# Kernel optimization log

Hardware: AMD Instinct MI355X
Metric: run time of the kernel (lower is better)

The kernel has to match this reference:

```python
import jax, jax.numpy as jnp
import numpy as np

B, L, H, E, MODES = 32, 2048, 8, 64, 64
SCALE = 1.0 / (512 * 512)  # 1/(in_channels*out_channels)


def setup_inputs() -> dict:
    key = jax.random.key(0)
    kq, kk, kv, kwr, kwi = jax.random.split(key, 5)
    # frequency mode selection: shuffled range(L//2), first MODES, sorted (get_frequency_modes)
    rng = np.random.default_rng(0)
    index = np.sort(rng.permutation(L // 2)[:MODES]).astype(np.int32)
    return {
        "q": jax.random.normal(kq, (B, L, H, E), dtype=jnp.float32),
        "k": jax.random.normal(kk, (B, L, H, E), dtype=jnp.float32),
        "v": jax.random.normal(kv, (B, L, H, E), dtype=jnp.float32),
        "w_real": SCALE * jax.random.uniform(kwr, (H, E, E, MODES), dtype=jnp.float32),
        "w_imag": SCALE * jax.random.uniform(kwi, (H, E, E, MODES), dtype=jnp.float32),
        "index": jnp.asarray(index),
    }


def reference(q, k, v, w_real, w_imag, index):
    # q: [B, L, H, E]; k, v unused by FourierBlock
    Bq, Lq, Hq, Eq = q.shape
    x = jnp.transpose(q, (0, 2, 3, 1))            # [B, H, E, L]
    x_ft = jnp.fft.rfft(x, axis=-1)               # [B, H, E, L//2+1] complex
    xs = jnp.take(x_ft, index, axis=-1)           # gather selected modes: [B, H, E, M]
    W = w_real + 1j * w_imag                      # [H, E, E, M] complex
    # vectorized per-mode complex einsum ('bhi,hio->bho' over all modes m)
    out = jnp.einsum('bhim,hiom->bhom', xs, W)    # [B, H, E, M]
    n_freq = Lq // 2 + 1
    # original writes mode wi into slot wi (0..M-1), rest stay zero
    out_ft = jnp.concatenate(
        [out, jnp.zeros((Bq, Hq, Eq, n_freq - out.shape[-1]), dtype=out.dtype)], axis=-1)
    return jnp.fft.irfft(out_ft, n=Lq, axis=-1)   # [B, H, E, L] real
```

## Files before the change

kernel.cpp:

```cpp
#include <hip/hip_runtime.h>
#include <math.h>

#define NB 32
#define NL 2048
#define NH 8
#define NE 64
#define NM 64
#define MRI 128
#define BK 128
#define NCH 16

typedef __attribute__((ext_vector_type(8))) __bf16 bf16x8;
typedef __attribute__((ext_vector_type(2))) __bf16 bf16x2;
typedef __attribute__((ext_vector_type(8))) unsigned short us8;
typedef __attribute__((ext_vector_type(4))) unsigned short us4;
typedef __attribute__((ext_vector_type(4))) float f32x4;
typedef __attribute__((ext_vector_type(16))) float f32x16;

__device__ __forceinline__ unsigned short f2bf(float x) {
  unsigned int u = __builtin_bit_cast(unsigned int, x);
  u = (u + 0x7fffu + ((u >> 16) & 1u)) >> 16;
  return (unsigned short)u;
}
__device__ __forceinline__ float bf2f(unsigned short u) {
  return __builtin_bit_cast(float, (unsigned int)u << 16);
}
__device__ __forceinline__ unsigned int pk2(float lo, float hi) {
  bf16x2 v;
  v[0] = (__bf16)lo;
  v[1] = (__bf16)hi;
  return __builtin_bit_cast(unsigned int, v);
}
__device__ __forceinline__ void gll16(const void* g, void* l) {
  __builtin_amdgcn_global_load_lds(
      (const __attribute__((address_space(1))) void*)g,
      (__attribute__((address_space(3))) void*)l, 16, 0, 0);
}

__global__ void tables_k(const int* __restrict__ idx,
                         const float* __restrict__ wr, const float* __restrict__ wi,
                         unsigned short* __restrict__ T, unsigned short* __restrict__ IT,
                         unsigned short* __restrict__ WBr, unsigned short* __restrict__ WBi) {
  int gid = blockIdx.x * blockDim.x + threadIdx.x;
  const float w0 = 6.283185307179586f / (float)NL;
  {
    int row = gid >> 11, l = gid & (NL - 1);
    int m = row & 63;
    int f = idx[m];
    float s, c;
    sincosf((float)((f * l) & (NL - 1)) * w0, &s, &c);
    T[gid] = f2bf(row < 64 ? c : -s);
  }
  {
    int lp = gid >> 7, k = gid & 127;
    int m = k & 63;
    float s, c;
    sincosf((float)((m * lp) & (NL - 1)) * w0, &s, &c);
    float v = (k < 64) ? ((m == 0 ? 1.0f : 2.0f) / (float)NL) * c
                       : (m == 0 ? 0.0f : (-2.0f / (float)NL) * s);
    IT[gid] = f2bf(v);
  }
  {
    const float2* wr2 = (const float2*)wr;
    const float2* wi2 = (const float2*)wi;
    unsigned int* obr = (unsigned int*)WBr;
    unsigned int* obi = (unsigned int*)WBi;
#pragma unroll
    for (int r = 0; r < 4; ++r) {
      int j = r * 262144 + gid;
      float2 a = wr2[j];
      float2 b2 = wi2[j];
      obr[j] = pk2(a.x, a.y);
      obi[j] = pk2(b2.x, b2.y);
    }
  }
}

__global__ __launch_bounds__(1024) void fused_k(const float* __restrict__ q,
                                                const unsigned short* __restrict__ T,
                                                const unsigned short* __restrict__ IT,
                                                const unsigned short* __restrict__ WBr,
                                                const unsigned short* __restrict__ WBi,
                                                float* __restrict__ out) {
  __shared__ __align__(16) char smem[99328];
  int t = threadIdx.x, lane = t & 63, wid = t >> 6;
  int h = blockIdx.x & 7, b = blockIdx.x >> 3;

  {
    char* Ab = smem;
    char* B0 = smem + 65536;
    char* B1 = smem + 65536 + 16896;
    const float* qb = q + ((size_t)b * NL * NH + h) * NE;
    int tm = wid & 3;
    int te = (wid >> 2) & 1;
    int kh = wid >> 3;
    int eq = t & 15, lq = t >> 4;
    f32x16 acc32 = {};
    f32x4 qA[2], qB[2];

    auto qload = [&](int c, f32x4* qr) {
#pragma unroll
      for (int p = 0; p < 2; ++p)
        qr[p] = *(const f32x4*)(qb + (size_t)(c * BK + lq * 2 + p) * (NH * NE) + eq * 4);
    };
    auto writesB = [&](const f32x4* qr, char* bb) {
#pragma unroll
      for (int j = 0; j < 4; ++j) {
        int e = eq * 4 + j;
        *(unsigned int*)(bb + e * 264 + lq * 4) = pk2(qr[0][j], qr[1][j]);
      }
    };
    auto stageA = [&](int bufi, int c) {
#pragma unroll
      for (int n = 0; n < 2; ++n) {
        int lin = n * 16384 + t * 16;
        int row = lin >> 8;
        int colb = (lin & 255) ^ ((row & 7) << 4);
        gll16((const char*)T + (size_t)row * (NL * 2) + (size_t)c * 256 + colb,
              Ab + bufi * 32768 + lin);
      }
    };
    auto compute = [&](const char* ab, const char* bb) {
#pragma unroll
      for (int ks = 0; ks < 4; ++ks) {
        int k0 = (kh * 4 + ks) * 16;
        int e = te * 32 + (lane & 31);
        int boff = e * 264 + (k0 + (lane >> 5) * 8) * 2;
        uint2 blo = *(const uint2*)(bb + boff);
        uint2 bhi = *(const uint2*)(bb + boff + 8);
        bf16x8 bfr = __builtin_bit_cast(bf16x8, make_uint4(blo.x, blo.y, bhi.x, bhi.y));
        int row = tm * 32 + (lane & 31);
        int aoff = (row * 256 + (k0 + (lane >> 5) * 8) * 2) ^ ((row & 7) << 4);
        bf16x8 afr = __builtin_bit_cast(bf16x8, *(const us8*)(ab + aoff));
        acc32 = __builtin_amdgcn_mfma_f32_32x32x16_bf16(afr, bfr, acc32, 0, 0, 0);
      }
    };

    qload(0, qA);
    qload(1, qB);
    stageA(0, 0);
    writesB(qA, B0);
    asm volatile("s_waitcnt vmcnt(0)" ::: "memory");
    __builtin_amdgcn_sched_barrier(0);
    asm volatile("s_waitcnt lgkmcnt(0)" ::: "memory");
    __builtin_amdgcn_s_barrier();
    for (int c = 0; c < 14; c += 2) {
      stageA(1, c + 1);
      qload(c + 2, qA);
      compute(Ab, B0);
      asm volatile("s_waitcnt vmcnt(2)" ::: "memory");
      __builtin_amdgcn_sched_barrier(0);
      __builtin_amdgcn_s_barrier();
      writesB(qB, B1);
      asm volatile("s_waitcnt lgkmcnt(0)" ::: "memory");
      __builtin_amdgcn_s_barrier();

      stageA(0, c + 2);
      qload(c + 3, qB);
      compute(Ab + 32768, B1);
      asm volatile("s_waitcnt vmcnt(2)" ::: "memory");
      __builtin_amdgcn_sched_barrier(0);
      __builtin_amdgcn_s_barrier();
      writesB(qA, B0);
      asm volatile("s_waitcnt lgkmcnt(0)" ::: "memory");
      __builtin_amdgcn_s_barrier();
    }
    stageA(1, 15);
    compute(Ab, B0);
    asm volatile("s_waitcnt vmcnt(0)" ::: "memory");
    __builtin_amdgcn_sched_barrier(0);
    __builtin_amdgcn_s_barrier();
    writesB(qB, B1);
    asm volatile("s_waitcnt lgkmcnt(0)" ::: "memory");
    __builtin_amdgcn_s_barrier();
    compute(Ab + 32768, B1);
    __syncthreads();

    float* scr = (float*)(smem + 65536);
    int tile = wid & 7;
    if (kh == 1) {
#pragma unroll
      for (int r = 0; r < 16; ++r) {
        int row = (r & 3) + 8 * (r >> 2) + 4 * (lane >> 5);
        scr[tile * 1024 + row * 32 + (lane & 31)] = acc32[r];
      }
    }
    __syncthreads();
    if (kh == 0) {
#pragma unroll
      for (int r = 0; r < 16; ++r) {
        int row = (r & 3) + 8 * (r >> 2) + 4 * (lane >> 5);
        float v = acc32[r] + scr[tile * 1024 + row * 32 + (lane & 31)];
        int grow = tm * 32 + row;
        int gcol = te * 32 + (lane & 31);
        int off = (grow * 272 + gcol * 4) ^ (((grow >> 3) & 7) << 4);
        *(float*)(smem + off) = v;
      }
    }
  }
  __syncthreads();

  {
    char* OtB = smem + 34816;
    int o = t >> 4, mq = t & 15;
    const unsigned short* wbr = WBr + (size_t)h * 262144 + o * 64 + mq * 4;
    const unsigned short* wbi = WBi + (size_t)h * 262144 + o * 64 + mq * 4;
    float orr[4] = {}, oii[4] = {};
#pragma unroll 2
    for (int ib = 0; ib < 16; ++ib) {
      f32x4 xr4[4], xi4[4];
#pragma unroll
      for (int mi = 0; mi < 4; ++mi) {
        int m = mq * 4 + mi;
        xr4[mi] = *(const f32x4*)(smem + ((m * 272 + ib * 16) ^ (((m >> 3) & 7) << 4)));
        xi4[mi] = *(const f32x4*)(smem + (((64 + m) * 272 + ib * 16) ^ (((m >> 3) & 7) << 4)));
      }
      us4 wr4[4], wi4[4];
#pragma unroll
      for (int ii = 0; ii < 4; ++ii) {
        int i = ib * 4 + ii;
        wr4[ii] = *(const us4*)(wbr + (size_t)i * 4096);
        wi4[ii] = *(const us4*)(wbi + (size_t)i * 4096);
      }
#pragma unroll
      for (int ii = 0; ii < 4; ++ii)
#pragma unroll
        for (int mi = 0; mi < 4; ++mi) {
          float wrv = bf2f(wr4[ii][mi]);
          float wiv = bf2f(wi4[ii][mi]);
          orr[mi] += xr4[mi][ii] * wrv - xi4[mi][ii] * wiv;
          oii[mi] += xr4[mi][ii] * wiv + xi4[mi][ii] * wrv;
        }
    }
    uint2 vr = make_uint2(pk2(orr[0], orr[1]), pk2(orr[2], orr[3]));
    uint2 vi = make_uint2(pk2(oii[0], oii[1]), pk2(oii[2], oii[3]));
    *(uint2*)(OtB + ((o * 256 + mq * 8) ^ ((o & 7) << 4))) = vr;
    *(uint2*)(OtB + ((o * 256 + 128 + mq * 8) ^ ((o & 7) << 4))) = vi;
  }
  __syncthreads();

  {
    const char* OtB = smem + 34816;
    bf16x8 af[2][8];
#pragma unroll
    for (int rg2 = 0; rg2 < 2; ++rg2)
#pragma unroll
      for (int ks = 0; ks < 8; ++ks) {
        int row = rg2 * 32 + (lane & 31);
        int off = (row * 256 + ks * 32 + (lane >> 5) * 16) ^ ((row & 7) << 4);
        af[rg2][ks] = __builtin_bit_cast(bf16x8, *(const us8*)(OtB + off));
      }
    float* ob = out + ((size_t)(b * 8 + h) * 64) * NL;
    int l0 = wid * 128;
    for (int ct = 0; ct < 4; ++ct) {
      int lr = l0 + ct * 32 + (lane & 31);
      f32x16 a2[2] = {};
#pragma unroll
      for (int ks = 0; ks < 8; ++ks) {
        bf16x8 bv = __builtin_bit_cast(
            bf16x8, *(const us8*)(IT + (size_t)lr * MRI + ks * 16 + (lane >> 5) * 8));
        a2[0] = __builtin_amdgcn_mfma_f32_32x32x16_bf16(af[0][ks], bv, a2[0], 0, 0, 0);
        a2[1] = __builtin_amdgcn_mfma_f32_32x32x16_bf16(af[1][ks], bv, a2[1], 0, 0, 0);
      }
#pragma unroll
      for (int rg2 = 0; rg2 < 2; ++rg2)
#pragma unroll
        for (int rg = 0; rg < 16; ++rg) {
          int row = rg2 * 32 + ((rg & 3) + 8 * (rg >> 2) + 4 * (lane >> 5));
          ob[(size_t)row * NL + lr] = a2[rg2][rg];
        }
    }
  }
}

extern "C" void kernel_launch(void* const* d_in, const int* in_sizes, int n_in,
                              void* d_out, int out_size, void* d_ws, size_t ws_size,
                              hipStream_t stream) {
  const float* q = (const float*)d_in[0];
  const float* wr = (const float*)d_in[3];
  const float* wi = (const float*)d_in[4];
  const int* idx = (const int*)d_in[5];
  float* out = (float*)d_out;
  char* ws = (char*)d_ws;

  constexpr size_t TBYTES = (size_t)MRI * NL * 2;
  constexpr size_t WBBYTES = (size_t)NH * NE * NE * NM * 2;
  constexpr size_t NEED = 2 * TBYTES + 2 * WBBYTES;
  if (ws_size < NEED) return;

  unsigned short* T = (unsigned short*)ws;
  unsigned short* IT = (unsigned short*)(ws + TBYTES);
  unsigned short* WBr = (unsigned short*)(ws + 2 * TBYTES);
  unsigned short* WBi = (unsigned short*)(ws + 2 * TBYTES + WBBYTES);

  hipLaunchKernelGGL(tables_k, dim3(1024), dim3(256), 0, stream, idx, wr, wi, T, IT, WBr, WBi);
  hipLaunchKernelGGL(fused_k, dim3(NB * NH), dim3(1024), 0, stream, q, T, IT, WBr, WBi, out);
}
```

Measured before the change: 85.36 us.

## Pre-swizzle DFT table into MFMA fragment order and load A into registers

```diff
diff --git a/kernel.cpp b/kernel.cpp
--- a/kernel.cpp
+++ b/kernel.cpp
@@ -31,25 +31,23 @@
   v[1] = (__bf16)hi;
   return __builtin_bit_cast(unsigned int, v);
 }
-__device__ __forceinline__ void gll16(const void* g, void* l) {
-  __builtin_amdgcn_global_load_lds(
-      (const __attribute__((address_space(1))) void*)g,
-      (__attribute__((address_space(3))) void*)l, 16, 0, 0);
-}
 
 __global__ void tables_k(const int* __restrict__ idx,
                          const float* __restrict__ wr, const float* __restrict__ wi,
-                         unsigned short* __restrict__ T, unsigned short* __restrict__ IT,
+                         unsigned short* __restrict__ Tf, unsigned short* __restrict__ IT,
                          unsigned short* __restrict__ WBr, unsigned short* __restrict__ WBi) {
   int gid = blockIdx.x * blockDim.x + threadIdx.x;
   const float w0 = 6.283185307179586f / (float)NL;
   {
-    int row = gid >> 11, l = gid & (NL - 1);
+    int j = gid & 7, lane_ = (gid >> 3) & 63, tm_ = (gid >> 9) & 3;
+    int ks_ = (gid >> 11) & 3, kh_ = (gid >> 13) & 1, c_ = gid >> 14;
+    int row = tm_ * 32 + (lane_ & 31);
     int m = row & 63;
+    int k = c_ * 128 + kh_ * 64 + ks_ * 16 + (lane_ >> 5) * 8 + j;
     int f = idx[m];
-    float s, c;
-    sincosf((float)((f * l) & (NL - 1)) * w0, &s, &c);
-    T[gid] = f2bf(row < 64 ? c : -s);
+    float s, c2;
+    sincosf((float)((f * k) & (NL - 1)) * w0, &s, &c2);
+    Tf[gid] = f2bf(row < 64 ? c2 : -s);
   }
   {
     int lp = gid >> 7, k = gid & 127;
@@ -82,14 +80,13 @@
                                                 const unsigned short* __restrict__ WBr,
                                                 const unsigned short* __restrict__ WBi,
                                                 float* __restrict__ out) {
-  __shared__ __align__(16) char smem[99328];
+  __shared__ __align__(16) char smem[84992];
   int t = threadIdx.x, lane = t & 63, wid = t >> 6;
   int h = blockIdx.x & 7, b = blockIdx.x >> 3;
 
   {
-    char* Ab = smem;
-    char* B0 = smem + 65536;
-    char* B1 = smem + 65536 + 16896;
+    char* B0 = smem + 51200;
+    char* B1 = smem + 51200 + 16896;
     const float* qb = q + ((size_t)b * NL * NH + h) * NE;
     int tm = wid & 3;
     int te = (wid >> 2) & 1;
@@ -97,6 +94,7 @@
     int eq = t & 15, lq = t >> 4;
     f32x16 acc32 = {};
     f32x4 qA[2], qB[2];
+    us8 arA[4], arB[4];
 
     auto qload = [&](int c, f32x4* qr) {
 #pragma unroll
@@ -110,17 +108,12 @@
         *(unsigned int*)(bb + e * 264 + lq * 4) = pk2(qr[0][j], qr[1][j]);
       }
     };
-    auto stageA = [&](int bufi, int c) {
-#pragma unroll
-      for (int n = 0; n < 2; ++n) {
-        int lin = n * 16384 + t * 16;
-        int row = lin >> 8;
-        int colb = (lin & 255) ^ ((row & 7) << 4);
-        gll16((const char*)T + (size_t)row * (NL * 2) + (size_t)c * 256 + colb,
-              Ab + bufi * 32768 + lin);
-      }
-    };
-    auto compute = [&](const char* ab, const char* bb) {
+    auto loadAreg = [&](int c, us8* ar) {
+#pragma unroll
+      for (int ks = 0; ks < 4; ++ks)
+        ar[ks] = *(const us8*)(T + ((((size_t)c * 2 + kh) * 4 + ks) * 4 + tm) * 512 + lane * 8);
+    };
+    auto compute = [&](const us8* ar, const char* bb) {
 #pragma unroll
       for (int ks = 0; ks < 4; ++ks) {
         int k0 = (kh * 4 + ks) * 16;
@@ -129,54 +122,38 @@
         uint2 blo = *(const uint2*)(bb + boff);
         uint2 bhi = *(const uint2*)(bb + boff + 8);
         bf16x8 bfr = __builtin_bit_cast(bf16x8, make_uint4(blo.x, blo.y, bhi.x, bhi.y));
-        int row = tm * 32 + (lane & 31);
-        int aoff = (row * 256 + (k0 + (lane >> 5) * 8) * 2) ^ ((row & 7) << 4);
-        bf16x8 afr = __builtin_bit_cast(bf16x8, *(const us8*)(ab + aoff));
-        acc32 = __builtin_amdgcn_mfma_f32_32x32x16_bf16(afr, bfr, acc32, 0, 0, 0);
+        acc32 = __builtin_amdgcn_mfma_f32_32x32x16_bf16(
+            __builtin_bit_cast(bf16x8, ar[ks]), bfr, acc32, 0, 0, 0);
       }
     };
 
     qload(0, qA);
     qload(1, qB);
-    stageA(0, 0);
+    loadAreg(0, arA);
     writesB(qA, B0);
-    asm volatile("s_waitcnt vmcnt(0)" ::: "memory");
-    __builtin_amdgcn_sched_barrier(0);
     asm volatile("s_waitcnt lgkmcnt(0)" ::: "memory");
     __builtin_amdgcn_s_barrier();
-    for (int c = 0; c < 14; c += 2) {
-      stageA(1, c + 1);
-      qload(c + 2, qA);
-      compute(Ab, B0);
-      asm volatile("s_waitcnt vmcnt(2)" ::: "memory");
-      __builtin_amdgcn_sched_barrier(0);
+    for (int c = 0; c < 16; c += 2) {
+      loadAreg(c + 1, arB);
+      if (c + 2 < 16) qload(c + 2, qA);
+      compute(arA, B0);
       __builtin_amdgcn_s_barrier();
       writesB(qB, B1);
       asm volatile("s_waitcnt lgkmcnt(0)" ::: "memory");
       __builtin_amdgcn_s_barrier();
-
-      stageA(0, c + 2);
-      qload(c + 3, qB);
-      compute(Ab + 32768, B1);
-      asm volatile("s_waitcnt vmcnt(2)" ::: "memory");
-      __builtin_amdgcn_sched_barrier(0);
-      __builtin_amdgcn_s_barrier();
-      writesB(qA, B0);
-      asm volatile("s_waitcnt lgkmcnt(0)" ::: "memory");
-      __builtin_amdgcn_s_barrier();
-    }
-    stageA(1, 15);
-    compute(Ab, B0);
-    asm volatile("s_waitcnt vmcnt(0)" ::: "memory");
-    __builtin_amdgcn_sched_barrier(0);
-    __builtin_amdgcn_s_barrier();
-    writesB(qB, B1);
-    asm volatile("s_waitcnt lgkmcnt(0)" ::: "memory");
-    __builtin_amdgcn_s_barrier();
-    compute(Ab + 32768, B1);
+      if (c + 2 < 16) loadAreg(c + 2, arA);
+      if (c + 3 < 16) qload(c + 3, qB);
+      compute(arB, B1);
+      if (c + 2 < 16) {
+        __builtin_amdgcn_s_barrier();
+        writesB(qA, B0);
+        asm volatile("s_waitcnt lgkmcnt(0)" ::: "memory");
+        __builtin_amdgcn_s_barrier();
+      }
+    }
     __syncthreads();
 
-    float* scr = (float*)(smem + 65536);
+    float* scr = (float*)(smem + 51200);
     int tile = wid & 7;
     if (kh == 1) {
 #pragma unroll
@@ -288,11 +265,11 @@
   constexpr size_t NEED = 2 * TBYTES + 2 * WBBYTES;
   if (ws_size < NEED) return;
 
-  unsigned short* T = (unsigned short*)ws;
+  unsigned short* Tf = (unsigned short*)ws;
   unsigned short* IT = (unsigned short*)(ws + TBYTES);
   unsigned short* WBr = (unsigned short*)(ws + 2 * TBYTES);
   unsigned short* WBi = (unsigned short*)(ws + 2 * TBYTES + WBBYTES);
 
-  hipLaunchKernelGGL(tables_k, dim3(1024), dim3(256), 0, stream, idx, wr, wi, T, IT, WBr, WBi);
-  hipLaunchKernelGGL(fused_k, dim3(NB * NH), dim3(1024), 0, stream, q, T, IT, WBr, WBi, out);
-}
+  hipLaunchKernelGGL(tables_k, dim3(1024), dim3(256), 0, stream, idx, wr, wi, Tf, IT, WBr, WBi);
+  hipLaunchKernelGGL(fused_k, dim3(NB * NH), dim3(1024), 0, stream, q, Tf, IT, WBr, WBi, out);
+}
```

Result: slower. 93.87 us (+10.0%).

## Split fused kernel into mode-halved DFT/mix kernel and tiled inverse-DFT GEMM kernel

Applied to the files above, without the earlier changes.

```diff
diff --git a/kernel.cpp b/kernel.cpp
--- a/kernel.cpp
+++ b/kernel.cpp
@@ -76,48 +76,49 @@
   }
 }
 
-__global__ __launch_bounds__(1024) void fused_k(const float* __restrict__ q,
+__global__ __launch_bounds__(512) void dftmix_k(const float* __restrict__ q,
                                                 const unsigned short* __restrict__ T,
-                                                const unsigned short* __restrict__ IT,
                                                 const unsigned short* __restrict__ WBr,
                                                 const unsigned short* __restrict__ WBi,
-                                                float* __restrict__ out) {
-  __shared__ __align__(16) char smem[99328];
+                                                unsigned short* __restrict__ O) {
+  __shared__ __align__(16) char smem[66560];
   int t = threadIdx.x, lane = t & 63, wid = t >> 6;
-  int h = blockIdx.x & 7, b = blockIdx.x >> 3;
-
-  {
-    char* Ab = smem;
-    char* B0 = smem + 65536;
-    char* B1 = smem + 65536 + 16896;
+  int h = blockIdx.x & 7, mh2 = (blockIdx.x >> 3) & 1, b = blockIdx.x >> 4;
+
+  {
+    char* A0 = smem;
+    char* A1 = smem + 16384;
+    char* B0 = smem + 32768;
+    char* B1 = smem + 32768 + 16896;
     const float* qb = q + ((size_t)b * NL * NH + h) * NE;
-    int tm = wid & 3;
-    int te = (wid >> 2) & 1;
-    int kh = wid >> 3;
-    int eq = t & 15, lq = t >> 4;
+    int tm = wid & 1;
+    int te = (wid >> 1) & 1;
+    int kh = wid >> 2;
+    int eq = t & 15, ls = t >> 4;
     f32x16 acc32 = {};
-    f32x4 qA[2], qB[2];
+    f32x4 qA[4], qB[4];
 
     auto qload = [&](int c, f32x4* qr) {
 #pragma unroll
-      for (int p = 0; p < 2; ++p)
-        qr[p] = *(const f32x4*)(qb + (size_t)(c * BK + lq * 2 + p) * (NH * NE) + eq * 4);
+      for (int p = 0; p < 4; ++p)
+        qr[p] = *(const f32x4*)(qb + (size_t)(c * BK + ls * 4 + p) * (NH * NE) + eq * 4);
     };
     auto writesB = [&](const f32x4* qr, char* bb) {
 #pragma unroll
       for (int j = 0; j < 4; ++j) {
         int e = eq * 4 + j;
-        *(unsigned int*)(bb + e * 264 + lq * 4) = pk2(qr[0][j], qr[1][j]);
+        *(uint2*)(bb + e * 264 + ls * 8) =
+            make_uint2(pk2(qr[0][j], qr[1][j]), pk2(qr[2][j], qr[3][j]));
       }
     };
-    auto stageA = [&](int bufi, int c) {
+    auto stageA = [&](char* ab, int c) {
 #pragma unroll
       for (int n = 0; n < 2; ++n) {
-        int lin = n * 16384 + t * 16;
-        int row = lin >> 8;
-        int colb = (lin & 255) ^ ((row & 7) << 4);
-        gll16((const char*)T + (size_t)row * (NL * 2) + (size_t)c * 256 + colb,
-              Ab + bufi * 32768 + lin);
+        int lin = n * 8192 + t * 16;
+        int rl = lin >> 8;
+        int grow = (rl < 32) ? (mh2 * 32 + rl) : (64 + mh2 * 32 + rl - 32);
+        int colb = (lin & 255) ^ ((rl & 7) << 4);
+        gll16((const char*)T + (size_t)grow * (NL * 2) + (size_t)c * 256 + colb, ab + lin);
       }
     };
     auto compute = [&](const char* ab, const char* bb) {
@@ -136,48 +137,46 @@
       }
     };
 
+    stageA(A0, 0);
     qload(0, qA);
     qload(1, qB);
-    stageA(0, 0);
     writesB(qA, B0);
-    asm volatile("s_waitcnt vmcnt(0)" ::: "memory");
-    __builtin_amdgcn_sched_barrier(0);
     asm volatile("s_waitcnt lgkmcnt(0)" ::: "memory");
     __builtin_amdgcn_s_barrier();
     for (int c = 0; c < 14; c += 2) {
-      stageA(1, c + 1);
+      stageA(A1, c + 1);
       qload(c + 2, qA);
-      compute(Ab, B0);
-      asm volatile("s_waitcnt vmcnt(2)" ::: "memory");
+      compute(A0, B0);
+      asm volatile("s_waitcnt vmcnt(4)" ::: "memory");
       __builtin_amdgcn_sched_barrier(0);
       __builtin_amdgcn_s_barrier();
       writesB(qB, B1);
       asm volatile("s_waitcnt lgkmcnt(0)" ::: "memory");
       __builtin_amdgcn_s_barrier();
 
-      stageA(0, c + 2);
-      qload(c + 3, qB);
-      compute(Ab + 32768, B1);
-      asm volatile("s_waitcnt vmcnt(2)" ::: "memory");
+      stageA(A0, c + 2);
+      if (c + 3 < 16) qload(c + 3, qB);
+      compute(A1, B1);
+      asm volatile("s_waitcnt vmcnt(4)" ::: "memory");
       __builtin_amdgcn_sched_barrier(0);
       __builtin_amdgcn_s_barrier();
       writesB(qA, B0);
       asm volatile("s_waitcnt lgkmcnt(0)" ::: "memory");
       __builtin_amdgcn_s_barrier();
     }
-    stageA(1, 15);
-    compute(Ab, B0);
+    stageA(A1, 15);
+    compute(A0, B0);
     asm volatile("s_waitcnt vmcnt(0)" ::: "memory");
     __builtin_amdgcn_sched_barrier(0);
     __builtin_amdgcn_s_barrier();
     writesB(qB, B1);
     asm volatile("s_waitcnt lgkmcnt(0)" ::: "memory");
     __builtin_amdgcn_s_barrier();
-    compute(Ab + 32768, B1);
+    compute(A1, B1);
     __syncthreads();
 
-    float* scr = (float*)(smem + 65536);
-    int tile = wid & 7;
+    float* scr = (float*)(smem + 32768);
+    int tile = wid & 3;
     if (kh == 1) {
 #pragma unroll
       for (int r = 0; r < 16; ++r) {
@@ -201,19 +200,20 @@
   __syncthreads();
 
   {
-    char* OtB = smem + 34816;
-    int o = t >> 4, mq = t & 15;
-    const unsigned short* wbr = WBr + (size_t)h * 262144 + o * 64 + mq * 4;
-    const unsigned short* wbi = WBi + (size_t)h * 262144 + o * 64 + mq * 4;
+    int o = t >> 3, mq = t & 7;
+    int mgbase = mh2 * 32 + mq * 4;
+    const unsigned short* wbr = WBr + (size_t)h * 262144 + o * 64 + mgbase;
+    const unsigned short* wbi = WBi + (size_t)h * 262144 + o * 64 + mgbase;
     float orr[4] = {}, oii[4] = {};
 #pragma unroll 2
     for (int ib = 0; ib < 16; ++ib) {
       f32x4 xr4[4], xi4[4];
 #pragma unroll
       for (int mi = 0; mi < 4; ++mi) {
-        int m = mq * 4 + mi;
-        xr4[mi] = *(const f32x4*)(smem + ((m * 272 + ib * 16) ^ (((m >> 3) & 7) << 4)));
-        xi4[mi] = *(const f32x4*)(smem + (((64 + m) * 272 + ib * 16) ^ (((m >> 3) & 7) << 4)));
+        int ml = mq * 4 + mi;
+        xr4[mi] = *(const f32x4*)(smem + ((ml * 272 + ib * 16) ^ (((ml >> 3) & 7) << 4)));
+        xi4[mi] = *(const f32x4*)(smem +
+                                  (((32 + ml) * 272 + ib * 16) ^ ((((32 + ml) >> 3) & 7) << 4)));
       }
       us4 wr4[4], wi4[4];
 #pragma unroll
@@ -232,45 +232,68 @@
           oii[mi] += xr4[mi][ii] * wiv + xi4[mi][ii] * wrv;
         }
     }
-    uint2 vr = make_uint2(pk2(orr[0], orr[1]), pk2(orr[2], orr[3]));
-    uint2 vi = make_uint2(pk2(oii[0], oii[1]), pk2(oii[2], oii[3]));
-    *(uint2*)(OtB + ((o * 256 + mq * 8) ^ ((o & 7) << 4))) = vr;
-    *(uint2*)(OtB + ((o * 256 + 128 + mq * 8) ^ ((o & 7) << 4))) = vi;
+    unsigned short* ob = O + (((size_t)b * 8 + h) * 64 + o) * MRI;
+    *(uint2*)(ob + mgbase) = make_uint2(pk2(orr[0], orr[1]), pk2(orr[2], orr[3]));
+    *(uint2*)(ob + 64 + mgbase) = make_uint2(pk2(oii[0], oii[1]), pk2(oii[2], oii[3]));
+  }
+}
+
+__global__ __launch_bounds__(256) void idft_k(const unsigned short* __restrict__ O,
+                                              const unsigned short* __restrict__ IT,
+                                              float* __restrict__ out) {
+  int bid = blockIdx.x;
+  int ct = bid & 15, rt = (bid >> 4) & 3, b = bid >> 6;
+  int t = threadIdx.x, lane = t & 63, wid = t >> 6;
+  __shared__ unsigned short Als[128 * 128];
+  __shared__ unsigned short Bls[128 * 128];
+  const unsigned short* Og = O + ((size_t)b * 512 + rt * 128) * MRI;
+  const unsigned short* Ig = IT + (size_t)ct * 128 * MRI;
+#pragma unroll
+  for (int n = 0; n < 8; ++n) {
+    int lin = n * 4096 + wid * 1024 + lane * 16;
+    int row = lin >> 8;
+    int colb = (lin & 255) ^ ((row & 7) << 4);
+    gll16((const char*)Og + (size_t)row * 256 + colb, (char*)Als + n * 4096 + wid * 1024);
+  }
+#pragma unroll
+  for (int n = 0; n < 8; ++n) {
+    int lin = n * 4096 + wid * 1024 + lane * 16;
+    int row = lin >> 8;
+    int colb = (lin & 255) ^ ((row & 7) << 4);
+    gll16((const char*)Ig + (size_t)row * 256 + colb, (char*)Bls + n * 4096 + wid * 1024);
   }
   __syncthreads();
-
-  {
-    const char* OtB = smem + 34816;
-    bf16x8 af[2][8];
-#pragma unroll
-    for (int rg2 = 0; rg2 < 2; ++rg2)
-#pragma unroll
-      for (int ks = 0; ks < 8; ++ks) {
-        int row = rg2 * 32 + (lane & 31);
-        int off = (row * 256 + ks * 32 + (lane >> 5) * 16) ^ ((row & 7) << 4);
-        af[rg2][ks] = __builtin_bit_cast(bf16x8, *(const us8*)(OtB + off));
-      }
-    float* ob = out + ((size_t)(b * 8 + h) * 64) * NL;
-    int l0 = wid * 128;
-    for (int ct = 0; ct < 4; ++ct) {
-      int lr = l0 + ct * 32 + (lane & 31);
-      f32x16 a2[2] = {};
-#pragma unroll
-      for (int ks = 0; ks < 8; ++ks) {
-        bf16x8 bv = __builtin_bit_cast(
-            bf16x8, *(const us8*)(IT + (size_t)lr * MRI + ks * 16 + (lane >> 5) * 8));
-        a2[0] = __builtin_amdgcn_mfma_f32_32x32x16_bf16(af[0][ks], bv, a2[0], 0, 0, 0);
-        a2[1] = __builtin_amdgcn_mfma_f32_32x32x16_bf16(af[1][ks], bv, a2[1], 0, 0, 0);
-      }
-#pragma unroll
-      for (int rg2 = 0; rg2 < 2; ++rg2)
-#pragma unroll
-        for (int rg = 0; rg < 16; ++rg) {
-          int row = rg2 * 32 + ((rg & 3) + 8 * (rg >> 2) + 4 * (lane >> 5));
-          ob[(size_t)row * NL + lr] = a2[rg2][rg];
-        }
-    }
-  }
+  int wr2 = (wid >> 1) * 64, wc = (wid & 1) * 64;
+  f32x16 acc[2][2] = {};
+#pragma unroll
+  for (int ksp = 0; ksp < 8; ++ksp) {
+    bf16x8 af[2], bfv[2];
+#pragma unroll
+    for (int i2 = 0; i2 < 2; ++i2) {
+      int row = wr2 + i2 * 32 + (lane & 31);
+      int off = ((row << 8) + (ksp << 5) + ((lane >> 5) << 4)) ^ ((row & 7) << 4);
+      af[i2] = __builtin_bit_cast(bf16x8, *(const us8*)((const char*)Als + off));
+      int nr = wc + i2 * 32 + (lane & 31);
+      int off2 = ((nr << 8) + (ksp << 5) + ((lane >> 5) << 4)) ^ ((nr & 7) << 4);
+      bfv[i2] = __builtin_bit_cast(bf16x8, *(const us8*)((const char*)Bls + off2));
+    }
+#pragma unroll
+    for (int i2 = 0; i2 < 2; ++i2)
+#pragma unroll
+      for (int j2 = 0; j2 < 2; ++j2)
+        acc[i2][j2] = __builtin_amdgcn_mfma_f32_32x32x16_bf16(af[i2], bfv[j2], acc[i2][j2], 0, 0, 0);
+  }
+  float* ob = out + ((size_t)b * 512 + rt * 128) * NL + ct * 128;
+#pragma unroll
+  for (int i2 = 0; i2 < 2; ++i2)
+#pragma unroll
+    for (int j2 = 0; j2 < 2; ++j2)
+#pragma unroll
+      for (int rg = 0; rg < 16; ++rg) {
+        int row = wr2 + i2 * 32 + ((rg & 3) + 8 * (rg >> 2) + 4 * (lane >> 5));
+        int col = wc + j2 * 32 + (lane & 31);
+        ob[(size_t)row * NL + col] = acc[i2][j2][rg];
+      }
 }
 
 extern "C" void kernel_launch(void* const* d_in, const int* in_sizes, int n_in,
@@ -285,14 +308,17 @@
 
   constexpr size_t TBYTES = (size_t)MRI * NL * 2;
   constexpr size_t WBBYTES = (size_t)NH * NE * NE * NM * 2;
-  constexpr size_t NEED = 2 * TBYTES + 2 * WBBYTES;
+  constexpr size_t OBYTES = (size_t)NB * NH * NE * MRI * 2;
+  constexpr size_t NEED = 2 * TBYTES + 2 * WBBYTES + OBYTES;
   if (ws_size < NEED) return;
 
   unsigned short* T = (unsigned short*)ws;
   unsigned short* IT = (unsigned short*)(ws + TBYTES);
   unsigned short* WBr = (unsigned short*)(ws + 2 * TBYTES);
   unsigned short* WBi = (unsigned short*)(ws + 2 * TBYTES + WBBYTES);
+  unsigned short* O = (unsigned short*)(ws + 2 * TBYTES + 2 * WBBYTES);
 
   hipLaunchKernelGGL(tables_k, dim3(1024), dim3(256), 0, stream, idx, wr, wi, T, IT, WBr, WBi);
-  hipLaunchKernelGGL(fused_k, dim3(NB * NH), dim3(1024), 0, stream, q, T, IT, WBr, WBi, out);
-}
+  hipLaunchKernelGGL(dftmix_k, dim3(512), dim3(512), 0, stream, q, T, WBr, WBi, O);
+  hipLaunchKernelGGL(idft_k, dim3(NB * 4 * 16), dim3(256), 0, stream, O, IT, out);
+}
```

Result: slower. 106.9 us (+25.3%).
